# Kernel optimization log

Hardware: AMD Instinct MI355X
Metric: run time of the kernel (lower is better)

The kernel has to match this reference:

```python
import jax, jax.numpy as jnp
import numpy as np

B, T, H = 4, 4096, 2048
NUM_HEADS, HEAD_DIM = 16, 128


def setup_inputs() -> dict:
    key = jax.random.key(0)
    k1, k2, k3 = jax.random.split(key, 3)
    hidden = jax.random.normal(k1, (B, T, H), dtype=jnp.float32)
    # Linear(H -> 3H): store weight as [H, 3H] for x @ W
    w_qkv = jax.random.normal(k2, (H, 3 * H), dtype=jnp.float32) * (1.0 / np.sqrt(H))
    b_qkv = jax.random.normal(k3, (3 * H,), dtype=jnp.float32) * 0.02
    return {"hidden": hidden, "w_qkv": w_qkv, "b_qkv": b_qkv}


def _to_heads(x):
    # (B, T, H) -> (B, num_heads, T, head_dim)
    b, t, _ = x.shape
    return x.reshape(b, t, NUM_HEADS, HEAD_DIM).transpose(0, 2, 1, 3)


def reference(hidden, w_qkv, b_qkv):
    # fused QKV projection: (B,T,H) @ (H,3H) + (3H,)
    qkv = jnp.einsum('bth,hd->btd', hidden, w_qkv) + b_qkv
    q, k, v = jnp.split(qkv, 3, axis=-1)
    return _to_heads(q), _to_heads(k), _to_heads(v)
```

## Files before the change

### kernel.cpp

```cpp
#include <hip/hip_runtime.h>
#include <hip/hip_bf16.h>
#include <stdint.h>

#define M_DIM 16384
#define K_DIM 2048
#define N_DIM 6144
#define NT    32
#define NTILES 6

typedef __attribute__((ext_vector_type(8))) short bf16x8;
typedef __attribute__((ext_vector_type(8))) unsigned short u16x8;
typedef __attribute__((ext_vector_type(4))) float f32x4;

__device__ __forceinline__ unsigned short f2bf(float f) {
  unsigned int u = __float_as_uint(f);
  u += 0x7FFFu + ((u >> 16) & 1u);
  return (unsigned short)(u >> 16);
}

__device__ __forceinline__ void load_lds16(const void* g, void* l) {
  __builtin_amdgcn_global_load_lds((const __attribute__((address_space(1))) void*)g,
                                   (__attribute__((address_space(3))) void*)l, 16, 0, 0);
}

#define FENCE asm volatile("" ::: "memory")
#define BAR   do { FENCE; __builtin_amdgcn_s_barrier(); FENCE; } while (0)
#define LGKM0 do { asm volatile("s_waitcnt lgkmcnt(0)" ::: "memory"); \
                   __builtin_amdgcn_sched_barrier(0); } while (0)

__global__ __launch_bounds__(256) void cvt_hidden(const float* __restrict__ in,
                                                  unsigned short* __restrict__ out) {
  unsigned int base = blockIdx.x * 256u + threadIdx.x;
  #pragma unroll
  for (int i = 0; i < 16; ++i) {
    unsigned int fi = i * 524288u + base;
    float4 v = reinterpret_cast<const float4*>(in)[fi];
    ushort4 o;
    o.x = f2bf(v.x); o.y = f2bf(v.y); o.z = f2bf(v.z); o.w = f2bf(v.w);
    reinterpret_cast<ushort4*>(out)[fi] = o;
  }
}

__global__ __launch_bounds__(256) void cvt_w(const float* __restrict__ w,
                                             unsigned short* __restrict__ wt) {
  __shared__ float tile[64][69];
  const int k0 = blockIdx.x * 64;
  const int n0 = blockIdx.y * 64;
  const int t = threadIdx.x;
  #pragma unroll
  for (int i = 0; i < 4; ++i) {
    int idx = i * 256 + t;
    int row = idx >> 4, c4 = idx & 15;
    float4 v = *reinterpret_cast<const float4*>(&w[(size_t)(k0 + row) * N_DIM + n0 + c4 * 4]);
    tile[row][c4 * 4 + 0] = v.x; tile[row][c4 * 4 + 1] = v.y;
    tile[row][c4 * 4 + 2] = v.z; tile[row][c4 * 4 + 3] = v.w;
  }
  __syncthreads();
  #pragma unroll
  for (int i = 0; i < 2; ++i) {
    int idx = i * 256 + t;
    int n = idx >> 3, k8 = idx & 7;
    u16x8 v;
    #pragma unroll
    for (int e = 0; e < 8; ++e) v[e] = f2bf(tile[k8 * 8 + e][n]);
    *reinterpret_cast<u16x8*>(&wt[(size_t)(n0 + n) * K_DIM + k0 + k8 * 8]) = v;
  }
}

__global__ __launch_bounds__(512, 2) void gemm_qkv_8ph(const unsigned short* __restrict__ A,
                                                       const unsigned short* __restrict__ Bt,
                                                       const float* __restrict__ bias,
                                                       float* __restrict__ out) {
  extern __shared__ __align__(16) char smem[];
  const int tid = threadIdx.x, lane = tid & 63, wid = tid >> 6;
  const int wm = wid >> 2, wn = wid & 3;

  const int xcd = blockIdx.x & 7;
  const int lcl = blockIdx.x >> 3;

  const int srow  = tid >> 3;
  const int sslot = (tid & 7) ^ ((tid >> 3) & 7);
  const int r15 = lane & 15, q4 = lane >> 4, x7 = lane & 7;
  const int abase = (wm * 128 + r15) * 128;
  const int bbase = (wn * 64  + r15) * 128;
  const int sw0 = ((0 + q4) ^ x7) * 16;
  const int sw1 = ((4 + q4) ^ x7) * 16;

  #define STAGE_T(gsrc, ldsbase)                                              \
    { const unsigned short* _g = (gsrc); char* _l = (ldsbase);                \
      load_lds16(_g,                       _l +     wid * 1024);              \
      load_lds16(_g + (size_t)64  * K_DIM, _l + 8192  + wid * 1024);          \
      load_lds16(_g + (size_t)128 * K_DIM, _l + 16384 + wid * 1024);          \
      load_lds16(_g + (size_t)192 * K_DIM, _l + 24576 + wid * 1024); }

  #define STAGE_H2(gsrc, ldsbase, cA, cB)                                     \
    { const unsigned short* _g = (gsrc); char* _l = (ldsbase);                \
      load_lds16(_g + (size_t)((cA) * 64) * K_DIM, _l + (cA) * 8192 + wid * 1024); \
      load_lds16(_g + (size_t)((cB) * 64) * K_DIM, _l + (cB) * 8192 + wid * 1024); }

  #define TILE_MAP(jj, m0_, n0_, gA_, gB_)                                    \
    { const int bm_ = xcd * 8 + (lcl >> 2);                                   \
      const int bn_ = (jj) * 4 + (lcl & 3);                                   \
      m0_ = bm_ * 256; n0_ = bn_ * 256;                                       \
      gA_ = A  + (size_t)(m0_ + srow) * K_DIM + sslot * 8;                    \
      gB_ = Bt + (size_t)(n0_ + srow) * K_DIM + sslot * 8; }

  if (tid < 384) {
    const int jj = tid / 64;
    const int o  = (tid & 63) * 4;
    const int bn_ = jj * 4 + (lcl & 3);
    f32x4 bv = *reinterpret_cast<const f32x4*>(&bias[bn_ * 256 + o]);
    *reinterpret_cast<f32x4*>(smem + 131072 + jj * 1024 + o * 4) = bv;
  }
  __builtin_amdgcn_sched_barrier(0);

  int m0, n0, m0n, n0n;
  const unsigned short *gA, *gB, *gAn, *gBn;
  TILE_MAP(0, m0, n0, gA, gB);
  {
    char* A0 = smem;          char* B0 = smem + 32768;
    char* A1 = smem + 65536;  char* B1 = smem + 98304;
    STAGE_T(gB +  0, B0); STAGE_T(gA +  0, A0);
    STAGE_T(gB + 64, B1); STAGE_T(gA + 64, A1);
    asm volatile("s_waitcnt vmcnt(8)" ::: "memory");
    BAR;
  }

  for (int j = 0; j < NTILES; ++j) {
    const int jn = (j + 1 < NTILES) ? j + 1 : j;
    TILE_MAP(jn, m0n, n0n, gAn, gBn);

    f32x4 acc[2][2][4][2] = {};
    bf16x8 a[4][2], b0[2][2], b1[2][2];

    for (int t = 0; t < NT; ++t) {
      char* Ab = smem + (t & 1) * 65536;
      char* Bb = Ab + 32768;
      const bool st = (t + 2 < NT) || (j + 1 < NTILES);
      const unsigned short* sA = (t + 2 < NT) ? gA + (size_t)(t + 2) * 64
                                              : gAn + (size_t)(t + 2 - NT) * 64;
      const unsigned short* sB = (t + 2 < NT) ? gB + (size_t)(t + 2) * 64
                                              : gBn + (size_t)(t + 2 - NT) * 64;

      #pragma unroll
      for (int mi = 0; mi < 4; ++mi) {
        const char* p = Ab + abase + mi * (16 * 128);
        a[mi][0] = *(const bf16x8*)(p + sw0);
        a[mi][1] = *(const bf16x8*)(p + sw1);
      }
      #pragma unroll
      for (int ni = 0; ni < 2; ++ni) {
        const char* p = Bb + bbase + ni * (16 * 128);
        b0[ni][0] = *(const bf16x8*)(p + sw0);
        b0[ni][1] = *(const bf16x8*)(p + sw1);
      }
      BAR; LGKM0;
      __builtin_amdgcn_s_setprio(1);
      #pragma unroll
      for (int mi = 0; mi < 4; ++mi)
        #pragma unroll
        for (int ni = 0; ni < 2; ++ni) {
          acc[0][0][mi][ni] = __builtin_amdgcn_mfma_f32_16x16x32_bf16(b0[ni][0], a[mi][0], acc[0][0][mi][ni], 0, 0, 0);
          acc[0][0][mi][ni] = __builtin_amdgcn_mfma_f32_16x16x32_bf16(b0[ni][1], a[mi][1], acc[0][0][mi][ni], 0, 0, 0);
        }
      __builtin_amdgcn_s_setprio(0);
      BAR;

      #pragma unroll
      for (int ni = 0; ni < 2; ++ni) {
        const char* p = Bb + bbase + (32 + ni * 16) * 128;
        b1[ni][0] = *(const bf16x8*)(p + sw0);
        b1[ni][1] = *(const bf16x8*)(p + sw1);
      }
      if (st) STAGE_H2(sA, Ab, 0, 2);
      BAR; LGKM0;
      __builtin_amdgcn_s_setprio(1);
      #pragma unroll
      for (int mi = 0; mi < 4; ++mi)
        #pragma unroll
        for (int ni = 0; ni < 2; ++ni) {
          acc[0][1][mi][ni] = __builtin_amdgcn_mfma_f32_16x16x32_bf16(b1[ni][0], a[mi][0], acc[0][1][mi][ni], 0, 0, 0);
          acc[0][1][mi][ni] = __builtin_amdgcn_mfma_f32_16x16x32_bf16(b1[ni][1], a[mi][1], acc[0][1][mi][ni], 0, 0, 0);
        }
      __builtin_amdgcn_s_setprio(0);
      BAR;

      #pragma unroll
      for (int mi = 0; mi < 4; ++mi) {
        const char* p = Ab + abase + (64 + mi * 16) * 128;
        a[mi][0] = *(const bf16x8*)(p + sw0);
        a[mi][1] = *(const bf16x8*)(p + sw1);
      }
      if (st) STAGE_H2(sB, Bb, 0, 1);
      BAR; LGKM0;
      __builtin_amdgcn_s_setprio(1);
      #pragma unroll
      for (int mi = 0; mi < 4; ++mi)
        #pragma unroll
        for (int ni = 0; ni < 2; ++ni) {
          acc[1][0][mi][ni] = __builtin_amdgcn_mfma_f32_16x16x32_bf16(b0[ni][0], a[mi][0], acc[1][0][mi][ni], 0, 0, 0);
          acc[1][0][mi][ni] = __builtin_amdgcn_mfma_f32_16x16x32_bf16(b0[ni][1], a[mi][1], acc[1][0][mi][ni], 0, 0, 0);
        }
      __builtin_amdgcn_s_setprio(0);
      BAR;

      if (st) { STAGE_H2(sB, Bb, 2, 3); STAGE_H2(sA, Ab, 1, 3); }
      BAR; LGKM0;
      __builtin_amdgcn_s_setprio(1);
      #pragma unroll
      for (int mi = 0; mi < 4; ++mi)
        #pragma unroll
        for (int ni = 0; ni < 2; ++ni) {
          acc[1][1][mi][ni] = __builtin_amdgcn_mfma_f32_16x16x32_bf16(b1[ni][0], a[mi][0], acc[1][1][mi][ni], 0, 0, 0);
          acc[1][1][mi][ni] = __builtin_amdgcn_mfma_f32_16x16x32_bf16(b1[ni][1], a[mi][1], acc[1][1][mi][ni], 0, 0, 0);
        }
      __builtin_amdgcn_s_setprio(0);
      if (t == 0 && j != 0)  { asm volatile("s_waitcnt vmcnt(40)" ::: "memory"); }
      else if (st)           { asm volatile("s_waitcnt vmcnt(6)"  ::: "memory"); }
      else                   { asm volatile("s_waitcnt vmcnt(0)"  ::: "memory"); }
      BAR;
    }

    const char* bl = smem + 131072 + j * 1024;
    f32x4 bq[2][2];
    #pragma unroll
    for (int qn = 0; qn < 2; ++qn)
      #pragma unroll
      for (int ni = 0; ni < 2; ++ni)
        bq[qn][ni] = *reinterpret_cast<const f32x4*>(
            bl + (wn * 64 + qn * 32 + ni * 16 + q4 * 4) * 4);

    #pragma unroll
    for (int qm = 0; qm < 2; ++qm)
      #pragma unroll
      for (int mi = 0; mi < 4; ++mi) {
        const int m = m0 + wm * 128 + qm * 64 + mi * 16 + r15;
        const int bb_ = m >> 12, tt = m & 4095;
        float* orow = out + (size_t)bb_ * 8388608 + (size_t)tt * 128;
        #pragma unroll
        for (int qn = 0; qn < 2; ++qn)
          #pragma unroll
          for (int ni = 0; ni < 2; ++ni) {
            const int col = n0 + wn * 64 + qn * 32 + ni * 16 + q4 * 4;
            const int which = col >> 11, head = (col & 2047) >> 7, hd = col & 127;
            f32x4 v = acc[qm][qn][mi][ni] + bq[qn][ni];
            __builtin_nontemporal_store(v,
                reinterpret_cast<f32x4*>(orow + (size_t)which * 33554432 +
                                         (size_t)head * 524288 + hd));
          }
      }

    m0 = m0n; n0 = n0n; gA = gAn; gB = gBn;
  }
  #undef STAGE_T
  #undef STAGE_H2
  #undef TILE_MAP
}

__global__ __launch_bounds__(256) void naive_qkv(const float* __restrict__ h,
                                                 const float* __restrict__ w,
                                                 const float* __restrict__ bias,
                                                 float* __restrict__ out) {
  const int m = blockIdx.x;
  const int n = blockIdx.y * 256 + threadIdx.x;
  const float* hr = h + (size_t)m * K_DIM;
  float acc = bias[n];
  for (int k = 0; k < K_DIM; ++k) acc = fmaf(hr[k], w[(size_t)k * N_DIM + n], acc);
  const int which = n >> 11, head = (n & 2047) >> 7, hd = n & 127;
  const int bb = m >> 12, tt = m & 4095;
  out[(size_t)which * 33554432 + (size_t)bb * 8388608 + (size_t)head * 524288 +
      (size_t)tt * 128 + hd] = acc;
}

extern "C" void kernel_launch(void* const* d_in, const int* in_sizes, int n_in,
                              void* d_out, int out_size, void* d_ws, size_t ws_size,
                              hipStream_t stream) {
  const float* hidden = (const float*)d_in[0];
  const float* w_qkv  = (const float*)d_in[1];
  const float* b_qkv  = (const float*)d_in[2];
  float* out = (float*)d_out;

  const size_t needA = (size_t)M_DIM * K_DIM * 2;
  const size_t needB = (size_t)N_DIM * K_DIM * 2;
  if (ws_size >= needA + needB) {
    unsigned short* Abf = (unsigned short*)d_ws;
    unsigned short* Wt  = (unsigned short*)((char*)d_ws + needA);
    (void)hipFuncSetAttribute((const void*)gemm_qkv_8ph,
                              hipFuncAttributeMaxDynamicSharedMemorySize, 137216);
    cvt_hidden<<<2048, 256, 0, stream>>>(hidden, Abf);
    cvt_w<<<dim3(32, 96), 256, 0, stream>>>(w_qkv, Wt);
    gemm_qkv_8ph<<<256, 512, 137216, stream>>>(Abf, Wt, b_qkv, out);
  } else {
    naive_qkv<<<dim3(16384, 24), 256, 0, stream>>>(hidden, w_qkv, b_qkv, out);
  }
}
```

Before: 445.1 us.

## Switch GEMM inner loop from 16x16x32 to 32x32x16 bf16 MFMA tiles

Replaces the 16x16x32 MFMA fragments with 32x32x16 MFMA instructions, reorganizing LDS fragment loads (32-row, 4 k-slices per lane half) and the accumulator layout to f32x16. The larger MFMA tile needs fewer LDS reads per flop and fewer instruction issues. The epilogue is rewritten to map the 32x32 output register layout to the head-split output with bias. The swizzled slot pattern changes too, so LDS bank conflicts may differ.

```diff
diff --git a/kernel.cpp b/kernel.cpp
--- a/kernel.cpp
+++ b/kernel.cpp
@@ -11,6 +11,7 @@
 typedef __attribute__((ext_vector_type(8))) short bf16x8;
 typedef __attribute__((ext_vector_type(8))) unsigned short u16x8;
 typedef __attribute__((ext_vector_type(4))) float f32x4;
+typedef __attribute__((ext_vector_type(16))) float f32x16;
 
 __device__ __forceinline__ unsigned short f2bf(float f) {
   unsigned int u = __float_as_uint(f);
@@ -80,11 +81,9 @@
 
   const int srow  = tid >> 3;
   const int sslot = (tid & 7) ^ ((tid >> 3) & 7);
-  const int r15 = lane & 15, q4 = lane >> 4, x7 = lane & 7;
-  const int abase = (wm * 128 + r15) * 128;
-  const int bbase = (wn * 64  + r15) * 128;
-  const int sw0 = ((0 + q4) ^ x7) * 16;
-  const int sw1 = ((4 + q4) ^ x7) * 16;
+  const int l31 = lane & 31, h = lane >> 5, x7 = lane & 7;
+  const int aq0 = (wm * 128 + l31) * 128;
+  const int bb  = (wn * 64  + l31) * 128;
 
   #define STAGE_T(gsrc, ldsbase)                                              \
     { const unsigned short* _g = (gsrc); char* _l = (ldsbase);                \
@@ -104,6 +103,8 @@
       m0_ = bm_ * 256; n0_ = bn_ * 256;                                       \
       gA_ = A  + (size_t)(m0_ + srow) * K_DIM + sslot * 8;                    \
       gB_ = Bt + (size_t)(n0_ + srow) * K_DIM + sslot * 8; }
+
+  #define SLOT(ks) ((((ks) * 2 + h) ^ x7) << 4)
 
   if (tid < 384) {
     const int jj = tid / 64;
@@ -130,8 +131,8 @@
     const int jn = (j + 1 < NTILES) ? j + 1 : j;
     TILE_MAP(jn, m0n, n0n, gAn, gBn);
 
-    f32x4 acc[2][2][4][2] = {};
-    bf16x8 a[4][2], b0[2][2], b1[2][2];
+    f32x16 acc[4][2] = {};
+    bf16x8 a[2][4], b0[4], b1[4];
 
     for (int t = 0; t < NT; ++t) {
       char* Ab = smem + (t & 1) * 65536;
@@ -143,64 +144,50 @@
                                               : gBn + (size_t)(t + 2 - NT) * 64;
 
       #pragma unroll
-      for (int mi = 0; mi < 4; ++mi) {
-        const char* p = Ab + abase + mi * (16 * 128);
-        a[mi][0] = *(const bf16x8*)(p + sw0);
-        a[mi][1] = *(const bf16x8*)(p + sw1);
-      }
-      #pragma unroll
-      for (int ni = 0; ni < 2; ++ni) {
-        const char* p = Bb + bbase + ni * (16 * 128);
-        b0[ni][0] = *(const bf16x8*)(p + sw0);
-        b0[ni][1] = *(const bf16x8*)(p + sw1);
-      }
-      BAR; LGKM0;
-      __builtin_amdgcn_s_setprio(1);
-      #pragma unroll
-      for (int mi = 0; mi < 4; ++mi)
-        #pragma unroll
-        for (int ni = 0; ni < 2; ++ni) {
-          acc[0][0][mi][ni] = __builtin_amdgcn_mfma_f32_16x16x32_bf16(b0[ni][0], a[mi][0], acc[0][0][mi][ni], 0, 0, 0);
-          acc[0][0][mi][ni] = __builtin_amdgcn_mfma_f32_16x16x32_bf16(b0[ni][1], a[mi][1], acc[0][0][mi][ni], 0, 0, 0);
-        }
-      __builtin_amdgcn_s_setprio(0);
-      BAR;
-
-      #pragma unroll
-      for (int ni = 0; ni < 2; ++ni) {
-        const char* p = Bb + bbase + (32 + ni * 16) * 128;
-        b1[ni][0] = *(const bf16x8*)(p + sw0);
-        b1[ni][1] = *(const bf16x8*)(p + sw1);
-      }
+      for (int mf = 0; mf < 2; ++mf)
+        #pragma unroll
+        for (int ks = 0; ks < 4; ++ks)
+          a[mf][ks] = *(const bf16x8*)(Ab + aq0 + mf * (32 * 128) + SLOT(ks));
+      #pragma unroll
+      for (int ks = 0; ks < 4; ++ks)
+        b0[ks] = *(const bf16x8*)(Bb + bb + SLOT(ks));
+      BAR; LGKM0;
+      __builtin_amdgcn_s_setprio(1);
+      #pragma unroll
+      for (int mf = 0; mf < 2; ++mf)
+        #pragma unroll
+        for (int ks = 0; ks < 4; ++ks)
+          acc[mf][0] = __builtin_amdgcn_mfma_f32_32x32x16_bf16(b0[ks], a[mf][ks], acc[mf][0], 0, 0, 0);
+      __builtin_amdgcn_s_setprio(0);
+      BAR;
+
+      #pragma unroll
+      for (int ks = 0; ks < 4; ++ks)
+        b1[ks] = *(const bf16x8*)(Bb + bb + 32 * 128 + SLOT(ks));
       if (st) STAGE_H2(sA, Ab, 0, 2);
       BAR; LGKM0;
       __builtin_amdgcn_s_setprio(1);
       #pragma unroll
-      for (int mi = 0; mi < 4; ++mi)
-        #pragma unroll
-        for (int ni = 0; ni < 2; ++ni) {
-          acc[0][1][mi][ni] = __builtin_amdgcn_mfma_f32_16x16x32_bf16(b1[ni][0], a[mi][0], acc[0][1][mi][ni], 0, 0, 0);
-          acc[0][1][mi][ni] = __builtin_amdgcn_mfma_f32_16x16x32_bf16(b1[ni][1], a[mi][1], acc[0][1][mi][ni], 0, 0, 0);
-        }
-      __builtin_amdgcn_s_setprio(0);
-      BAR;
-
-      #pragma unroll
-      for (int mi = 0; mi < 4; ++mi) {
-        const char* p = Ab + abase + (64 + mi * 16) * 128;
-        a[mi][0] = *(const bf16x8*)(p + sw0);
-        a[mi][1] = *(const bf16x8*)(p + sw1);
-      }
+      for (int mf = 0; mf < 2; ++mf)
+        #pragma unroll
+        for (int ks = 0; ks < 4; ++ks)
+          acc[mf][1] = __builtin_amdgcn_mfma_f32_32x32x16_bf16(b1[ks], a[mf][ks], acc[mf][1], 0, 0, 0);
+      __builtin_amdgcn_s_setprio(0);
+      BAR;
+
+      #pragma unroll
+      for (int mf = 0; mf < 2; ++mf)
+        #pragma unroll
+        for (int ks = 0; ks < 4; ++ks)
+          a[mf][ks] = *(const bf16x8*)(Ab + aq0 + (64 + mf * 32) * 128 + SLOT(ks));
       if (st) STAGE_H2(sB, Bb, 0, 1);
       BAR; LGKM0;
       __builtin_amdgcn_s_setprio(1);
       #pragma unroll
-      for (int mi = 0; mi < 4; ++mi)
-        #pragma unroll
-        for (int ni = 0; ni < 2; ++ni) {
-          acc[1][0][mi][ni] = __builtin_amdgcn_mfma_f32_16x16x32_bf16(b0[ni][0], a[mi][0], acc[1][0][mi][ni], 0, 0, 0);
-          acc[1][0][mi][ni] = __builtin_amdgcn_mfma_f32_16x16x32_bf16(b0[ni][1], a[mi][1], acc[1][0][mi][ni], 0, 0, 0);
-        }
+      for (int mf = 0; mf < 2; ++mf)
+        #pragma unroll
+        for (int ks = 0; ks < 4; ++ks)
+          acc[2 + mf][0] = __builtin_amdgcn_mfma_f32_32x32x16_bf16(b0[ks], a[mf][ks], acc[2 + mf][0], 0, 0, 0);
       __builtin_amdgcn_s_setprio(0);
       BAR;
 
@@ -208,12 +195,10 @@
       BAR; LGKM0;
       __builtin_amdgcn_s_setprio(1);
       #pragma unroll
-      for (int mi = 0; mi < 4; ++mi)
-        #pragma unroll
-        for (int ni = 0; ni < 2; ++ni) {
-          acc[1][1][mi][ni] = __builtin_amdgcn_mfma_f32_16x16x32_bf16(b1[ni][0], a[mi][0], acc[1][1][mi][ni], 0, 0, 0);
-          acc[1][1][mi][ni] = __builtin_amdgcn_mfma_f32_16x16x32_bf16(b1[ni][1], a[mi][1], acc[1][1][mi][ni], 0, 0, 0);
-        }
+      for (int mf = 0; mf < 2; ++mf)
+        #pragma unroll
+        for (int ks = 0; ks < 4; ++ks)
+          acc[2 + mf][1] = __builtin_amdgcn_mfma_f32_32x32x16_bf16(b1[ks], a[mf][ks], acc[2 + mf][1], 0, 0, 0);
       __builtin_amdgcn_s_setprio(0);
       if (t == 0 && j != 0)  { asm volatile("s_waitcnt vmcnt(40)" ::: "memory"); }
       else if (st)           { asm volatile("s_waitcnt vmcnt(6)"  ::: "memory"); }
@@ -222,39 +207,42 @@
     }
 
     const char* bl = smem + 131072 + j * 1024;
-    f32x4 bq[2][2];
+    f32x4 bq[2][4];
     #pragma unroll
-    for (int qn = 0; qn < 2; ++qn)
-      #pragma unroll
-      for (int ni = 0; ni < 2; ++ni)
-        bq[qn][ni] = *reinterpret_cast<const f32x4*>(
-            bl + (wn * 64 + qn * 32 + ni * 16 + q4 * 4) * 4);
+    for (int nf = 0; nf < 2; ++nf)
+      #pragma unroll
+      for (int rg = 0; rg < 4; ++rg)
+        bq[nf][rg] = *reinterpret_cast<const f32x4*>(
+            bl + (wn * 64 + nf * 32 + rg * 8 + 4 * h) * 4);
 
     #pragma unroll
-    for (int qm = 0; qm < 2; ++qm)
-      #pragma unroll
-      for (int mi = 0; mi < 4; ++mi) {
-        const int m = m0 + wm * 128 + qm * 64 + mi * 16 + r15;
-        const int bb_ = m >> 12, tt = m & 4095;
-        float* orow = out + (size_t)bb_ * 8388608 + (size_t)tt * 128;
-        #pragma unroll
-        for (int qn = 0; qn < 2; ++qn)
-          #pragma unroll
-          for (int ni = 0; ni < 2; ++ni) {
-            const int col = n0 + wn * 64 + qn * 32 + ni * 16 + q4 * 4;
-            const int which = col >> 11, head = (col & 2047) >> 7, hd = col & 127;
-            f32x4 v = acc[qm][qn][mi][ni] + bq[qn][ni];
-            __builtin_nontemporal_store(v,
-                reinterpret_cast<f32x4*>(orow + (size_t)which * 33554432 +
-                                         (size_t)head * 524288 + hd));
-          }
-      }
+    for (int mf = 0; mf < 4; ++mf) {
+      const int m = m0 + wm * 128 + mf * 32 + l31;
+      const int bb_ = m >> 12, tt = m & 4095;
+      float* orow = out + (size_t)bb_ * 8388608 + (size_t)tt * 128;
+      #pragma unroll
+      for (int nf = 0; nf < 2; ++nf)
+        #pragma unroll
+        for (int rg = 0; rg < 4; ++rg) {
+          const int col = n0 + wn * 64 + nf * 32 + rg * 8 + 4 * h;
+          const int which = col >> 11, head = (col & 2047) >> 7, hd = col & 127;
+          f32x4 v;
+          v[0] = acc[mf][nf][rg * 4 + 0] + bq[nf][rg][0];
+          v[1] = acc[mf][nf][rg * 4 + 1] + bq[nf][rg][1];
+          v[2] = acc[mf][nf][rg * 4 + 2] + bq[nf][rg][2];
+          v[3] = acc[mf][nf][rg * 4 + 3] + bq[nf][rg][3];
+          __builtin_nontemporal_store(v,
+              reinterpret_cast<f32x4*>(orow + (size_t)which * 33554432 +
+                                       (size_t)head * 524288 + hd));
+        }
+    }
 
     m0 = m0n; n0 = n0n; gA = gAn; gB = gBn;
   }
   #undef STAGE_T
   #undef STAGE_H2
   #undef TILE_MAP
+  #undef SLOT
 }
 
 __global__ __launch_bounds__(256) void naive_qkv(const float* __restrict__ h,
```

Result: slower. 677.5 us (+52.2%).
